# Optimization experiments

Measured on AMD Instinct MI355X. Metric: run time of the kernel, lower is better.

The kernel has to match this reference:

```python
import jax, jax.numpy as jnp
import numpy as np

EMBED_DIM = 768
NUM_HEADS = 12
HEAD_DIM = EMBED_DIM // NUM_HEADS


def setup_inputs() -> dict:
    key = jax.random.key(0)
    ks = jax.random.split(key, 5)
    B, N, D = 8, 1024, EMBED_DIM
    s = 1.0 / np.sqrt(D)
    x = jax.random.normal(ks[0], (B, N, D), dtype=jnp.float32)
    W_qkv = jax.random.normal(ks[1], (D, 3 * D), dtype=jnp.float32) * s
    b_qkv = jnp.zeros((3 * D,), dtype=jnp.float32)
    W_proj = jax.random.normal(ks[2], (D, D), dtype=jnp.float32) * s
    b_proj = jnp.zeros((D,), dtype=jnp.float32)
    return {"x": x, "W_qkv": W_qkv, "b_qkv": b_qkv, "W_proj": W_proj, "b_proj": b_proj}


def reference(x, W_qkv, b_qkv, W_proj, b_proj):
    B, N, D = x.shape
    H, Hd = NUM_HEADS, HEAD_DIM
    scale = Hd ** -0.5
    qkv = x @ W_qkv + b_qkv                      # (B, N, 3D)
    qkv = qkv.reshape(B, N, 3, H, Hd).transpose(2, 0, 3, 1, 4)  # (3, B, H, N, Hd)
    q, k, v = qkv[0], qkv[1], qkv[2]
    attn = jnp.einsum('bhnd,bhmd->bhnm', q, k) * scale  # (B, H, N, N)
    attn = jax.nn.softmax(attn, axis=-1)
    out = jnp.einsum('bhnm,bhmd->bhnd', attn, v)        # (B, H, N, Hd)
    out = out.transpose(0, 2, 1, 3).reshape(B, N, D)
    return out @ W_proj + b_proj
```

## Files before the change

### kernel.cpp

```cpp
#include <hip/hip_runtime.h>


#define B_   8
#define N_   1024
#define D_   768
#define H_   12
#define HD_  64

typedef __attribute__((ext_vector_type(4))) float f32x4;
typedef __attribute__((ext_vector_type(16))) float f32x16;
typedef __attribute__((ext_vector_type(8))) short bf16x8;
typedef __attribute__((ext_vector_type(2))) unsigned int u32x2;
typedef __attribute__((ext_vector_type(4))) unsigned int u32x4;

__device__ __forceinline__ unsigned short f2bf(float f) {
    unsigned int u = __float_as_uint(f);
    u += 0x7fff + ((u >> 16) & 1);
    return (unsigned short)(u >> 16);
}
__device__ __forceinline__ unsigned int pk2(float a, float b) {
    return (unsigned int)f2bf(a) | ((unsigned int)f2bf(b) << 16);
}
__device__ __forceinline__ unsigned int pk2t(float a, float b) {
    return __builtin_amdgcn_perm(__float_as_uint(b), __float_as_uint(a), 0x07060302u);
}
__device__ __forceinline__ float truncbf(float f) {
    return __uint_as_float(__float_as_uint(f) & 0xFFFF0000u);
}
__device__ __forceinline__ void gl_lds16(const void* g, void* l) {
    __builtin_amdgcn_global_load_lds(
        (const __attribute__((address_space(1))) unsigned int*)g,
        (__attribute__((address_space(3))) unsigned int*)l, 16, 0, 0);
}
#define MFMA(a, b, c)   __builtin_amdgcn_mfma_f32_16x16x32_bf16(a, b, c, 0, 0, 0)
#define MFMA32(a, b, c) __builtin_amdgcn_mfma_f32_32x32x16_bf16(a, b, c, 0, 0, 0)
#define BAR() do { __asm__ volatile("" ::: "memory"); \
    __builtin_amdgcn_s_barrier(); \
    __asm__ volatile("" ::: "memory"); } while (0)
#define WAITVM(n) do { __asm__ volatile("" ::: "memory"); \
    __builtin_amdgcn_s_waitcnt(0xF70 | (n)); \
    __asm__ volatile("" ::: "memory"); } while (0)
#define WAITLGKM() __asm__ volatile("s_waitcnt lgkmcnt(0)" ::: "memory")

__global__ __launch_bounds__(256) void prep_kernel(
    const float* __restrict__ x, const float* __restrict__ wqkv,
    const float* __restrict__ wproj,
    unsigned short* __restrict__ XB, unsigned short* __restrict__ WQT,
    unsigned short* __restrict__ WPT)
{
    const int bid = blockIdx.x;
    const int tid = threadIdx.x;
    if (bid < 3072) {
        int id = bid * 256 + tid;
        int r  = id & 127;
        int kc = (id >> 7) & 7;
        int ks = (id >> 10) % 12;
        int nt = id / 12288;
        const float* src = x + (size_t)(nt * 128 + r) * 768 + ks * 64 + kc * 8;
        float4 f0 = *(const float4*)src;
        float4 f1 = *(const float4*)(src + 4);
        uint4 o;
        o.x = pk2(f0.x, f0.y); o.y = pk2(f0.z, f0.w);
        o.z = pk2(f1.x, f1.y); o.w = pk2(f1.z, f1.w);
        *(uint4*)&XB[(size_t)id * 8] = o;
    } else if (bid < 3936) {
        int id = (bid - 3072) * 256 + tid;
        int fr = id & 127;
        int kc = (id >> 7) & 7;
        int ks = (id >> 10) % 12;
        int mt = id / 12288;
        float v[8];
#pragma unroll
        for (int j = 0; j < 8; ++j)
            v[j] = wqkv[(size_t)(ks * 64 + kc * 8 + j) * 2304 + mt * 128 + fr];
        uint4 o;
        o.x = pk2(v[0], v[1]); o.y = pk2(v[2], v[3]);
        o.z = pk2(v[4], v[5]); o.w = pk2(v[6], v[7]);
        *(uint4*)&WQT[(size_t)id * 8] = o;
    } else {
        int id = (bid - 3936) * 256 + tid;
        int fr = id & 63;
        int kc = (id >> 6) & 7;
        int ks = (id >> 9) % 12;
        int nt = id / 6144;
        float v[8];
#pragma unroll
        for (int j = 0; j < 8; ++j)
            v[j] = wproj[(size_t)(ks * 64 + kc * 8 + j) * 768 + nt * 64 + fr];
        uint4 o;
        o.x = pk2(v[0], v[1]); o.y = pk2(v[2], v[3]);
        o.z = pk2(v[4], v[5]); o.w = pk2(v[6], v[7]);
        *(uint4*)&WPT[(size_t)id * 8] = o;
    }
}

__global__ __launch_bounds__(256, 4) void qkv_gemm(
    const unsigned short* __restrict__ XB,
    const unsigned short* __restrict__ WQT,
    const float* __restrict__ bias,
    unsigned short* __restrict__ QS,
    unsigned short* __restrict__ KS,
    unsigned short* __restrict__ VS)
{
    __shared__ __align__(16) unsigned short sm[16384];

    const int tid = threadIdx.x;
    const int w = tid >> 6, lane = tid & 63;
    const int l15 = lane & 15, quad = lane >> 4;
    const int mt = blockIdx.x >> 6;
    const int nt = blockIdx.x & 63;
    const int m0w = (w & 1) * 64, n0w = (w >> 1) * 64;
    const float CS = 0.18033688f;

    char* smb = (char*)sm;
    const char* baseA = (const char*)(WQT + (size_t)(mt * 12) * 8192);
    const char* baseB = (const char*)(XB  + (size_t)(nt * 12) * 8192);

    auto issue = [&](int ks) {
        const char* sA = baseA + ks * 8192;
        const char* sB = baseB + ks * 8192;
        const int pb = ks & 1;
#pragma unroll
        for (int i = 0; i < 2; ++i) {
            const int c = w * 2 + i;
            gl_lds16(sA + (c * 64 + lane) * 16, smb + pb * 8192 + c * 1024);
            gl_lds16(sB + (c * 64 + lane) * 16, smb + 16384 + pb * 8192 + c * 1024);
        }
    };

    f32x4 acc[4][4];
    const f32x4 z = {0.f, 0.f, 0.f, 0.f};
#pragma unroll
    for (int t = 0; t < 4; ++t)
#pragma unroll
        for (int u = 0; u < 4; ++u) acc[t][u] = z;

    issue(0);
    for (int ks = 0; ks < 24; ++ks) {
        BAR();
        if (ks < 23) { issue(ks + 1); WAITVM(4); } else { WAITVM(0); }
        BAR();
        const unsigned short* Ab = sm + (ks & 1) * 4096;
        const unsigned short* Bb = sm + 8192 + (ks & 1) * 4096;
        bf16x8 af[4], bfv[4];
#pragma unroll
        for (int t = 0; t < 4; ++t)
            af[t] = *(const bf16x8*)(Ab + (quad * 128 + m0w + t * 16 + l15) * 8);
#pragma unroll
        for (int u = 0; u < 4; ++u)
            bfv[u] = *(const bf16x8*)(Bb + (quad * 128 + n0w + u * 16 + l15) * 8);
#pragma unroll
        for (int t = 0; t < 4; ++t)
#pragma unroll
            for (int u = 0; u < 4; ++u)
                acc[t][u] = MFMA(af[t], bfv[u], acc[t][u]);
    }

    const int part = mt / 6;
    BAR();

#pragma unroll
    for (int t = 0; t < 4; ++t) {
        int d = m0w + t * 16 + quad * 4;
        float4 bv = *(const float4*)&bias[part * 768 + (mt % 6) * 128 + d];
#pragma unroll
        for (int u = 0; u < 4; ++u) {
            int tok = n0w + u * 16 + l15;
            f32x4 a = acc[t][u];
            float v0 = a[0] + bv.x, v1 = a[1] + bv.y;
            float v2 = a[2] + bv.z, v3 = a[3] + bv.w;
            if (part == 0) { v0 *= CS; v1 *= CS; v2 *= CS; v3 *= CS; }
            if (part < 2) {
                unsigned off = tok * 256 + (((unsigned)(d * 2)) ^ ((tok & 7) << 4));
                uint2 pp; pp.x = pk2(v0, v1); pp.y = pk2(v2, v3);
                *(uint2*)(smb + off) = pp;
            } else {
                float vv[4] = {v0, v1, v2, v3};
#pragma unroll
                for (int r4 = 0; r4 < 4; ++r4) {
                    int dd = d + r4;
                    unsigned off = dd * 256 + (((unsigned)(tok * 2)) ^ ((dd & 7) << 4));
                    *(unsigned short*)(smb + off) = f2bf(vv[r4]);
                }
            }
        }
    }
    BAR();

    const int b = nt >> 3, qtc = nt & 7;
    if (part == 0) {
#pragma unroll
        for (int round = 0; round < 8; ++round) {
            int r = tid & 127;
            int kc = (tid >> 7) + round * 2;
            uint4 val = *(const uint4*)(smb + r * 256 +
                        (((unsigned)(kc << 4)) ^ ((r & 7) << 4)));
            int h = (mt % 6) * 2 + (kc >> 3);
            int bh = b * H_ + h;
            *(uint4*)(QS + (((size_t)(bh * 8 + qtc) * 1024) + (kc & 7) * 128 + r) * 8) = val;
        }
    } else if (part == 1) {
#pragma unroll
        for (int round = 0; round < 8; ++round) {
            int r = tid & 127;
            int kc = (tid >> 7) + round * 2;
            uint4 val = *(const uint4*)(smb + r * 256 +
                        (((unsigned)(kc << 4)) ^ ((r & 7) << 4)));
            int h = (mt % 6) * 2 + (kc >> 3);
            int bh = b * H_ + h;
            int kt = (qtc << 1) | (r >> 6);
            *(uint4*)(KS + (((size_t)(bh * 16 + kt) * 512) + (kc & 7) * 64 + (r & 63)) * 8) = val;
        }
    } else {
#pragma unroll
        for (int round = 0; round < 8; ++round) {
            int dd = tid & 127;
            int tc = (tid >> 7) + round * 2;
            uint4 val = *(const uint4*)(smb + dd * 256 +
                        (((unsigned)(tc << 4)) ^ ((dd & 7) << 4)));
            int h = (mt % 6) * 2 + (dd >> 6);
            int bh = b * H_ + h;
            int kt = (qtc << 1) | (tc >> 3);
            *(uint4*)(VS + (((size_t)(bh * 16 + kt) * 512) + (tc & 7) * 64 + (dd & 63)) * 8) = val;
        }
    }
}

__global__ __launch_bounds__(256, 3) void attn_kernel(
    const unsigned short* __restrict__ QS,
    const unsigned short* __restrict__ KS,
    const unsigned short* __restrict__ VS,
    unsigned short* __restrict__ AWS)
{
    __shared__ __align__(16) unsigned short sm[24576];
    const int tid = threadIdx.x;
    const int w = tid >> 6, lane = tid & 63;
    const int l31 = lane & 31, h = lane >> 5;
    const int bh = blockIdx.x % 96;
    const int qt = blockIdx.x / 96;

    char* smb = (char*)sm;
    const char* kbase = (const char*)(KS + (size_t)(bh * 16) * 4096);
    const char* vbase = (const char*)(VS + (size_t)(bh * 16) * 4096);

    auto issue_tile = [&](int kt) {
        const char* ks_ = kbase + kt * 8192;
        const char* vs_ = vbase + kt * 8192;
        const int sl = kt % 3;
#pragma unroll
        for (int i = 0; i < 2; ++i) {
            const int c = w * 2 + i;
            gl_lds16(ks_ + (c * 64 + lane) * 16, smb + sl * 8192 + c * 1024);
            gl_lds16(vs_ + (c * 64 + lane) * 16, smb + 24576 + sl * 8192 + c * 1024);
        }
    };

    const char* qslab = (const char*)(QS + (size_t)(bh * 8 + qt) * 8192);
#pragma unroll
    for (int i = 0; i < 4; ++i) {
        const int c = w * 4 + i;
        char* dst = (c < 8) ? (smb + 16384 + c * 1024)
                            : (smb + 40960 + (c - 8) * 1024);
        gl_lds16(qslab + (c * 64 + lane) * 16, dst);
    }
    issue_tile(0);
    issue_tile(1);

    WAITVM(8);
    BAR();
    bf16x8 qf[4];
#pragma unroll
    for (int ks = 0; ks < 4; ++ks) {
        const char* qreg = (ks < 2) ? (smb + 16384) : (smb + 40960);
        const int dcl = (ks & 1) * 2 + h;
        qf[ks] = *(const bf16x8*)(qreg + (dcl * 128 + w * 32 + l31) * 16);
    }
    WAITLGKM();

    f32x16 acc[2];
    const f32x16 z16 = {0.f,0.f,0.f,0.f,0.f,0.f,0.f,0.f,
                        0.f,0.f,0.f,0.f,0.f,0.f,0.f,0.f};
    acc[0] = z16; acc[1] = z16;
    float lsum = 0.f;

    for (int kt = 0; kt < 16; ++kt) {
        BAR();
        if (kt < 14)      { issue_tile(kt + 2); WAITVM(8); }
        else if (kt == 14){ WAITVM(4); }
        else              { WAITVM(0); }
        BAR();
        const char* Kb = smb + (kt % 3) * 8192;
        const char* Vb = smb + 24576 + (kt % 3) * 8192;

        f32x16 sv[2] = {z16, z16};
        __builtin_amdgcn_s_setprio(1);
#pragma unroll
        for (int ks = 0; ks < 4; ++ks) {
#pragma unroll
            for (int kb = 0; kb < 2; ++kb) {
                bf16x8 kf = *(const bf16x8*)(Kb +
                            ((ks * 2 + h) * 64 + kb * 32 + l31) * 16);
                sv[kb] = MFMA32(kf, qf[ks], sv[kb]);
            }
        }
        __builtin_amdgcn_s_setprio(0);

        unsigned pw[4][4];
#pragma unroll
        for (int kb = 0; kb < 2; ++kb) {
            float p[16];
#pragma unroll
            for (int r = 0; r < 16; ++r)
                p[r] = truncbf(__builtin_amdgcn_exp2f(sv[kb][r]));
            lsum += ((((p[0] + p[1]) + (p[2] + p[3])) +
                      ((p[4] + p[5]) + (p[6] + p[7]))) +
                     (((p[8] + p[9]) + (p[10] + p[11])) +
                      ((p[12] + p[13]) + (p[14] + p[15]))));
            unsigned X0 = pk2t(p[0],  p[1]),  X1 = pk2t(p[2],  p[3]);
            unsigned Y0 = pk2t(p[4],  p[5]),  Y1 = pk2t(p[6],  p[7]);
            unsigned Z0 = pk2t(p[8],  p[9]),  Z1 = pk2t(p[10], p[11]);
            unsigned W0 = pk2t(p[12], p[13]), W1 = pk2t(p[14], p[15]);
            u32x2 a0 = __builtin_amdgcn_permlane32_swap(X0, Y0, false, false);
            u32x2 a1 = __builtin_amdgcn_permlane32_swap(X1, Y1, false, false);
            u32x2 b0 = __builtin_amdgcn_permlane32_swap(Z0, W0, false, false);
            u32x2 b1 = __builtin_amdgcn_permlane32_swap(Z1, W1, false, false);
            pw[kb * 2][0] = a0[0]; pw[kb * 2][1] = a1[0];
            pw[kb * 2][2] = a0[1]; pw[kb * 2][3] = a1[1];
            pw[kb * 2 + 1][0] = b0[0]; pw[kb * 2 + 1][1] = b1[0];
            pw[kb * 2 + 1][2] = b0[1]; pw[kb * 2 + 1][3] = b1[1];
        }

        __builtin_amdgcn_s_setprio(1);
#pragma unroll
        for (int ks = 0; ks < 4; ++ks) {
            u32x4 pv = {pw[ks][0], pw[ks][1], pw[ks][2], pw[ks][3]};
            bf16x8 pf = __builtin_bit_cast(bf16x8, pv);
#pragma unroll
            for (int db = 0; db < 2; ++db) {
                bf16x8 vf = *(const bf16x8*)(Vb +
                            ((ks * 2 + h) * 64 + db * 32 + l31) * 16);
                acc[db] = MFMA32(vf, pf, acc[db]);
            }
        }
        __builtin_amdgcn_s_setprio(0);
    }

    float lfull = lsum + __shfl_xor(lsum, 32, 64);
    float inv = 1.f / lfull;

    const int b = bh / H_, hh = bh % H_;
    const int mtA = b * 8 + qt;
    unsigned short* obase = AWS + (size_t)(mtA * 12 + hh) * 8192;
#pragma unroll
    for (int db = 0; db < 2; ++db) {
#pragma unroll
        for (int gp = 0; gp < 2; ++gp) {
            const int g0 = gp * 2, g1 = gp * 2 + 1;
            unsigned v00 = pk2(acc[db][4 * g0 + 0] * inv, acc[db][4 * g0 + 1] * inv);
            unsigned v01 = pk2(acc[db][4 * g0 + 2] * inv, acc[db][4 * g0 + 3] * inv);
            unsigned v10 = pk2(acc[db][4 * g1 + 0] * inv, acc[db][4 * g1 + 1] * inv);
            unsigned v11 = pk2(acc[db][4 * g1 + 2] * inv, acc[db][4 * g1 + 3] * inv);
            u32x2 t0 = __builtin_amdgcn_permlane32_swap(v00, v10, false, false);
            u32x2 t1 = __builtin_amdgcn_permlane32_swap(v01, v11, false, false);
            uint4 val;
            val.x = t0[0]; val.y = t1[0]; val.z = t0[1]; val.w = t1[1];
            const int dc = db * 4 + g0 + h;
            *(uint4*)(obase + ((size_t)(dc * 128) + w * 32 + l31) * 8) = val;
        }
    }
}

__global__ __launch_bounds__(256, 3) void proj_gemm(
    const unsigned short* __restrict__ AWS,
    const unsigned short* __restrict__ WPT,
    const float* __restrict__ bias, float* __restrict__ out)
{
    __shared__ __align__(16) unsigned short As[2][8192];
    __shared__ __align__(16) unsigned short Bs[2][4096];

    const int tid = threadIdx.x;
    const int w = tid >> 6, lane = tid & 63;
    const int l15 = lane & 15, quad = lane >> 4;
    const int mt = blockIdx.x / 12;
    const int nt = blockIdx.x % 12;
    const int m0w = (w & 1) * 64, n0w = (w >> 1) * 32;

    const char* baseA = (const char*)(AWS + (size_t)(mt * 12) * 8192);
    const char* baseB = (const char*)(WPT + (size_t)(nt * 12) * 4096);

    auto issue = [&](int ks) {
        const char* sA = baseA + ks * 16384;
        const char* sB = baseB + ks * 8192;
        const int pb = ks & 1;
#pragma unroll
        for (int i = 0; i < 4; ++i) {
            const int c = w * 4 + i;
            gl_lds16(sA + (c * 64 + lane) * 16, (char*)As + pb * 16384 + c * 1024);
        }
#pragma unroll
        for (int i = 0; i < 2; ++i) {
            const int c = w * 2 + i;
            gl_lds16(sB + (c * 64 + lane) * 16, (char*)Bs + pb * 8192 + c * 1024);
        }
    };

    f32x4 acc[4][2];
    const f32x4 z = {0.f, 0.f, 0.f, 0.f};
#pragma unroll
    for (int t = 0; t < 4; ++t) { acc[t][0] = z; acc[t][1] = z; }

    issue(0);
    for (int ks = 0; ks < 12; ++ks) {
        BAR();
        if (ks < 11) { issue(ks + 1); WAITVM(6); } else { WAITVM(0); }
        BAR();
        const unsigned short* Ab = As[ks & 1];
        const unsigned short* Bb = Bs[ks & 1];
#pragma unroll
        for (int kk = 0; kk < 2; ++kk) {
            bf16x8 af[4], bfv[2];
#pragma unroll
            for (int t = 0; t < 4; ++t)
                af[t] = *(const bf16x8*)(Ab + (((kk * 4 + quad) * 128) + m0w + t * 16 + l15) * 8);
#pragma unroll
            for (int u = 0; u < 2; ++u)
                bfv[u] = *(const bf16x8*)(Bb + (((kk * 4 + quad) * 64) + n0w + u * 16 + l15) * 8);
#pragma unroll
            for (int t = 0; t < 4; ++t)
#pragma unroll
                for (int u = 0; u < 2; ++u)
                    acc[t][u] = MFMA(af[t], bfv[u], acc[t][u]);
        }
    }

#pragma unroll
    for (int t = 0; t < 4; ++t)
#pragma unroll
        for (int u = 0; u < 2; ++u) {
            int col = nt * 64 + n0w + u * 16 + l15;
            float bvv = bias[col];
#pragma unroll
            for (int r = 0; r < 4; ++r) {
                int row = mt * 128 + m0w + t * 16 + quad * 4 + r;
                out[(size_t)row * 768 + col] = acc[t][u][r] + bvv;
            }
        }
}

extern "C" void kernel_launch(void* const* d_in, const int* in_sizes, int n_in,
                              void* d_out, int out_size, void* d_ws, size_t ws_size,
                              hipStream_t stream) {
    const float* x     = (const float*)d_in[0];
    const float* Wqkv  = (const float*)d_in[1];
    const float* bqkv  = (const float*)d_in[2];
    const float* Wproj = (const float*)d_in[3];
    const float* bproj = (const float*)d_in[4];
    float* out = (float*)d_out;

    unsigned short* ws = (unsigned short*)d_ws;
    unsigned short* XB  = ws;
    unsigned short* WQT = ws + 6291456;
    unsigned short* WPT = ws + 8060928;
    unsigned short* QS  = ws + 8650752;
    unsigned short* KS  = ws + 14942208;
    unsigned short* VS  = ws + 21233664;
    unsigned short* AWS = ws + 27525120;

    prep_kernel<<<dim3(4224), dim3(256), 0, stream>>>(x, Wqkv, Wproj, XB, WQT, WPT);
    qkv_gemm<<<dim3(18 * 64), dim3(256), 0, stream>>>(XB, WQT, bqkv, QS, KS, VS);
    attn_kernel<<<dim3(96 * 8), dim3(256), 0, stream>>>(QS, KS, VS, AWS);
    proj_gemm<<<dim3(64 * 12), dim3(256), 0, stream>>>(AWS, WPT, bproj, out);
}
```

Baseline: 176.8 us.

## Load Q and V straight to registers, double-buffer only K in LDS

```diff
diff --git a/kernel.cpp b/kernel.cpp
--- a/kernel.cpp
+++ b/kernel.cpp
@@ -232,7 +232,7 @@
     const unsigned short* __restrict__ VS,
     unsigned short* __restrict__ AWS)
 {
-    __shared__ __align__(16) unsigned short sm[24576];
+    __shared__ __align__(16) unsigned short sm[8192];
     const int tid = threadIdx.x;
     const int w = tid >> 6, lane = tid & 63;
     const int l31 = lane & 31, h = lane >> 5;
@@ -243,39 +243,24 @@
     const char* kbase = (const char*)(KS + (size_t)(bh * 16) * 4096);
     const char* vbase = (const char*)(VS + (size_t)(bh * 16) * 4096);
 
-    auto issue_tile = [&](int kt) {
+    auto issue_k = [&](int kt) {
         const char* ks_ = kbase + kt * 8192;
-        const char* vs_ = vbase + kt * 8192;
-        const int sl = kt % 3;
+        const int sl = kt & 1;
 #pragma unroll
         for (int i = 0; i < 2; ++i) {
             const int c = w * 2 + i;
             gl_lds16(ks_ + (c * 64 + lane) * 16, smb + sl * 8192 + c * 1024);
-            gl_lds16(vs_ + (c * 64 + lane) * 16, smb + 24576 + sl * 8192 + c * 1024);
         }
     };
 
     const char* qslab = (const char*)(QS + (size_t)(bh * 8 + qt) * 8192);
-#pragma unroll
-    for (int i = 0; i < 4; ++i) {
-        const int c = w * 4 + i;
-        char* dst = (c < 8) ? (smb + 16384 + c * 1024)
-                            : (smb + 40960 + (c - 8) * 1024);
-        gl_lds16(qslab + (c * 64 + lane) * 16, dst);
-    }
-    issue_tile(0);
-    issue_tile(1);
-
-    WAITVM(8);
-    BAR();
     bf16x8 qf[4];
 #pragma unroll
-    for (int ks = 0; ks < 4; ++ks) {
-        const char* qreg = (ks < 2) ? (smb + 16384) : (smb + 40960);
-        const int dcl = (ks & 1) * 2 + h;
-        qf[ks] = *(const bf16x8*)(qreg + (dcl * 128 + w * 32 + l31) * 16);
-    }
-    WAITLGKM();
+    for (int ks = 0; ks < 4; ++ks)
+        qf[ks] = *(const bf16x8*)(qslab +
+                 (((ks * 2 + h) * 128) + w * 32 + l31) * 16);
+    issue_k(0);
+    issue_k(1);
 
     f32x16 acc[2];
     const f32x16 z16 = {0.f,0.f,0.f,0.f,0.f,0.f,0.f,0.f,
@@ -284,13 +269,18 @@
     float lsum = 0.f;
 
     for (int kt = 0; kt < 16; ++kt) {
+        WAITVM(0);
         BAR();
-        if (kt < 14)      { issue_tile(kt + 2); WAITVM(8); }
-        else if (kt == 14){ WAITVM(4); }
-        else              { WAITVM(0); }
-        BAR();
-        const char* Kb = smb + (kt % 3) * 8192;
-        const char* Vb = smb + 24576 + (kt % 3) * 8192;
+        const char* Kb = smb + (kt & 1) * 8192;
+
+        const char* vt = vbase + kt * 8192;
+        bf16x8 vfr[4][2];
+#pragma unroll
+        for (int ks = 0; ks < 4; ++ks)
+#pragma unroll
+            for (int db = 0; db < 2; ++db)
+                vfr[ks][db] = *(const bf16x8*)(vt +
+                              (((ks * 2 + h) * 64) + db * 32 + l31) * 16);
 
         f32x16 sv[2] = {z16, z16};
         __builtin_amdgcn_s_setprio(1);
@@ -304,6 +294,8 @@
             }
         }
         __builtin_amdgcn_s_setprio(0);
+
+        if (kt < 15) issue_k(kt + 1);
 
         unsigned pw[4][4];
 #pragma unroll
@@ -336,11 +328,8 @@
             u32x4 pv = {pw[ks][0], pw[ks][1], pw[ks][2], pw[ks][3]};
             bf16x8 pf = __builtin_bit_cast(bf16x8, pv);
 #pragma unroll
-            for (int db = 0; db < 2; ++db) {
-                bf16x8 vf = *(const bf16x8*)(Vb +
-                            ((ks * 2 + h) * 64 + db * 32 + l31) * 16);
-                acc[db] = MFMA32(vf, pf, acc[db]);
-            }
+            for (int db = 0; db < 2; ++db)
+                acc[db] = MFMA32(vfr[ks][db], pf, acc[db]);
         }
         __builtin_amdgcn_s_setprio(0);
     }
```

Measured after the change: 176.7 us. About the same (-0.1%).

## Use one barrier per iteration and load Q straight into registers

Applied to the files above, without the earlier changes.

```diff
diff --git a/kernel.cpp b/kernel.cpp
--- a/kernel.cpp
+++ b/kernel.cpp
@@ -23,9 +23,6 @@
 }
 __device__ __forceinline__ unsigned int pk2t(float a, float b) {
     return __builtin_amdgcn_perm(__float_as_uint(b), __float_as_uint(a), 0x07060302u);
-}
-__device__ __forceinline__ float truncbf(float f) {
-    return __uint_as_float(__float_as_uint(f) & 0xFFFF0000u);
 }
 __device__ __forceinline__ void gl_lds16(const void* g, void* l) {
     __builtin_amdgcn_global_load_lds(
@@ -40,7 +37,6 @@
 #define WAITVM(n) do { __asm__ volatile("" ::: "memory"); \
     __builtin_amdgcn_s_waitcnt(0xF70 | (n)); \
     __asm__ volatile("" ::: "memory"); } while (0)
-#define WAITLGKM() __asm__ volatile("s_waitcnt lgkmcnt(0)" ::: "memory")
 
 __global__ __launch_bounds__(256) void prep_kernel(
     const float* __restrict__ x, const float* __restrict__ wqkv,
@@ -136,10 +132,10 @@
         for (int u = 0; u < 4; ++u) acc[t][u] = z;
 
     issue(0);
+    WAITVM(0);
+    BAR();
     for (int ks = 0; ks < 24; ++ks) {
-        BAR();
-        if (ks < 23) { issue(ks + 1); WAITVM(4); } else { WAITVM(0); }
-        BAR();
+        if (ks < 23) issue(ks + 1);
         const unsigned short* Ab = sm + (ks & 1) * 4096;
         const unsigned short* Bb = sm + 8192 + (ks & 1) * 4096;
         bf16x8 af[4], bfv[4];
@@ -154,6 +150,7 @@
 #pragma unroll
             for (int u = 0; u < 4; ++u)
                 acc[t][u] = MFMA(af[t], bfv[u], acc[t][u]);
+        if (ks < 23) { WAITVM(0); BAR(); }
     }
 
     const int part = mt / 6;
@@ -256,26 +253,16 @@
     };
 
     const char* qslab = (const char*)(QS + (size_t)(bh * 8 + qt) * 8192);
-#pragma unroll
-    for (int i = 0; i < 4; ++i) {
-        const int c = w * 4 + i;
-        char* dst = (c < 8) ? (smb + 16384 + c * 1024)
-                            : (smb + 40960 + (c - 8) * 1024);
-        gl_lds16(qslab + (c * 64 + lane) * 16, dst);
-    }
+    bf16x8 qf[4];
+#pragma unroll
+    for (int ks = 0; ks < 4; ++ks)
+        qf[ks] = *(const bf16x8*)(qslab +
+                 (((ks * 2 + h) * 128) + w * 32 + l31) * 16);
+
     issue_tile(0);
     issue_tile(1);
-
-    WAITVM(8);
+    WAITVM(4);
     BAR();
-    bf16x8 qf[4];
-#pragma unroll
-    for (int ks = 0; ks < 4; ++ks) {
-        const char* qreg = (ks < 2) ? (smb + 16384) : (smb + 40960);
-        const int dcl = (ks & 1) * 2 + h;
-        qf[ks] = *(const bf16x8*)(qreg + (dcl * 128 + w * 32 + l31) * 16);
-    }
-    WAITLGKM();
 
     f32x16 acc[2];
     const f32x16 z16 = {0.f,0.f,0.f,0.f,0.f,0.f,0.f,0.f,
@@ -284,11 +271,6 @@
     float lsum = 0.f;
 
     for (int kt = 0; kt < 16; ++kt) {
-        BAR();
-        if (kt < 14)      { issue_tile(kt + 2); WAITVM(8); }
-        else if (kt == 14){ WAITVM(4); }
-        else              { WAITVM(0); }
-        BAR();
         const char* Kb = smb + (kt % 3) * 8192;
         const char* Vb = smb + 24576 + (kt % 3) * 8192;
 
@@ -311,7 +293,7 @@
             float p[16];
 #pragma unroll
             for (int r = 0; r < 16; ++r)
-                p[r] = truncbf(__builtin_amdgcn_exp2f(sv[kb][r]));
+                p[r] = __builtin_amdgcn_exp2f(sv[kb][r]);
             lsum += ((((p[0] + p[1]) + (p[2] + p[3])) +
                       ((p[4] + p[5]) + (p[6] + p[7]))) +
                      (((p[8] + p[9]) + (p[10] + p[11])) +
@@ -343,6 +325,9 @@
             }
         }
         __builtin_amdgcn_s_setprio(0);
+
+        if (kt < 14)       { issue_tile(kt + 2); WAITVM(4); BAR(); }
+        else if (kt == 14) { WAITVM(0); BAR(); }
     }
 
     float lfull = lsum + __shfl_xor(lsum, 32, 64);
@@ -410,10 +395,10 @@
     for (int t = 0; t < 4; ++t) { acc[t][0] = z; acc[t][1] = z; }
 
     issue(0);
+    WAITVM(0);
+    BAR();
     for (int ks = 0; ks < 12; ++ks) {
-        BAR();
-        if (ks < 11) { issue(ks + 1); WAITVM(6); } else { WAITVM(0); }
-        BAR();
+        if (ks < 11) issue(ks + 1);
         const unsigned short* Ab = As[ks & 1];
         const unsigned short* Bb = Bs[ks & 1];
 #pragma unroll
@@ -431,6 +416,7 @@
                 for (int u = 0; u < 2; ++u)
                     acc[t][u] = MFMA(af[t], bfv[u], acc[t][u]);
         }
+        if (ks < 11) { WAITVM(0); BAR(); }
     }
 
 #pragma unroll
```

New measurement: 181.2 us. 2.5% more time.
